# Performance work log

Measured on AMD Instinct MI355X. Metric: run time of the kernel, lower is better.

Reference implementation:

```python
import jax, jax.numpy as jnp
import numpy as np

N, G, H = 262144, 512, 16
EPS = 1e-5

Q_MAT = jnp.array([[0.0, 0.0, 1.0], [1.0, 0.0, 0.0], [0.0, 1.0, 0.0]], dtype=jnp.float32)
Q_TENSOR = jnp.kron(Q_MAT, Q_MAT)  # 9x9


def setup_inputs() -> dict:
    key = jax.random.key(0)
    ks = jax.random.split(key, 10)
    # sorted node->graph ids, every graph guaranteed non-empty
    gid = jnp.sort(jnp.concatenate([
        jnp.arange(G, dtype=jnp.int32),
        jax.random.randint(ks[0], (N - G,), 0, G, dtype=jnp.int32)]))
    return {
        'x00': jax.random.normal(ks[1], (N, 4 * H), jnp.float32),
        'x10': jax.random.normal(ks[2], (N, H, 3), jnp.float32),
        'x01': jax.random.normal(ks[3], (N, H, 3), jnp.float32),
        'x11': jax.random.normal(ks[4], (N, H, 9), jnp.float32),
        'pos': jax.random.normal(ks[5], (N, 6), jnp.float32),
        'graph_ids': gid,
        'num_graphs': G,
        'bn_gamma': jnp.ones((4 * H,), jnp.float32),
        'bn_beta': jnp.zeros((4 * H,), jnp.float32),
        'lin_w': jax.random.normal(ks[6], (3, 4 * H), jnp.float32) * 0.1,
        'lin_b': jnp.zeros((3,), jnp.float32),
        'w10': jax.random.normal(ks[7], (1, H), jnp.float32) * 0.3,
        'w01': jax.random.normal(ks[8], (1, H), jnp.float32) * 0.3,
        'w11': jax.random.normal(ks[9], (1, H), jnp.float32) * 0.3,
    }


def _graph_norm(x, seg, num_seg, gamma, beta):
    # per-graph mean/var normalization over nodes ('gn')
    cnt = jax.ops.segment_sum(jnp.ones((x.shape[0],), x.dtype), seg, num_segments=num_seg)
    cnt = jnp.maximum(cnt, 1.0)[:, None]
    mean = jax.ops.segment_sum(x, seg, num_segments=num_seg) / cnt
    var = jax.ops.segment_sum(x * x, seg, num_segments=num_seg) / cnt - mean * mean
    xn = (x - mean[seg]) * jax.lax.rsqrt(var[seg] + EPS)
    return xn * gamma + beta


def _segment_softmax(logits, seg, num_seg):
    m = jax.ops.segment_max(logits, seg, num_segments=num_seg)
    e = jnp.exp(logits - m[seg])
    s = jax.ops.segment_sum(e, seg, num_segments=num_seg)
    return e / s[seg]


def _project_r(r_vector):
    # SVD projection to nearest rotation (sign-corrected)
    norm = jnp.clip(jnp.linalg.norm(r_vector, axis=1, keepdims=True), 1e-5, None)
    r_vector = r_vector / jax.lax.stop_gradient(norm)  # norm is detached in torch
    # einops 'b (d c) -> b c d' with c=3
    r_ = jnp.transpose(r_vector.reshape(-1, 3, 3), (0, 2, 1))
    U, S, Vh = jnp.linalg.svd(r_, full_matrices=False)
    rot_pos = U @ Vh
    Vh_neg = Vh.at[:, 2, :].multiply(-1.0)
    rot_neg = U @ Vh_neg
    det = jnp.linalg.det(rot_pos)
    return jnp.where(det[:, None, None] > 0, rot_pos, rot_neg)


def reference(x00, x10, x01, x11, pos, graph_ids, num_graphs,
              bn_gamma, bn_beta, lin_w, lin_b, w10, w01, w11):
    seg = graph_ids
    Gn = num_graphs
    # BN('gn') + Linear -> 3 per-node logits
    xn = _graph_norm(x00, seg, Gn, bn_gamma, bn_beta)
    logits = xn @ lin_w.T + lin_b                       # [N,3]
    W = _segment_softmax(logits, seg, Gn)                # per-graph softmax over nodes
    w0, w1, w2 = W[:, 0:1], W[:, 1:2], W[:, 2:3]
    # weighted per-graph sums (dgl.sum_nodes)
    ab = jnp.concatenate([x10, x01], axis=-1)            # [N,H,6]
    mean_ab = jax.ops.segment_sum(ab * w1[:, :, None], seg, num_segments=Gn)   # [G,H,6]
    r_sum = jax.ops.segment_sum(x11 * w0[:, :, None], seg, num_segments=Gn)    # [G,H,9]
    m1m2 = jax.ops.segment_sum(pos * w2, seg, num_segments=Gn)                 # [G,6]
    m1, m2 = m1m2[:, 0:3], m1m2[:, 3:]
    # GLinear head: channel-mixing H -> 1 per degree type (no bias)
    out10 = jnp.einsum('oc,gcd->god', w10, mean_ab[:, :, :3])[:, 0, :]  # [G,3]
    out01 = jnp.einsum('oc,gcd->god', w01, mean_ab[:, :, 3:6])[:, 0, :]
    out11 = jnp.einsum('oc,gcd->god', w11, r_sum)[:, 0, :]              # [G,9]
    # permutation back to input frame
    r_vector = jnp.einsum('ij,gj->gi', Q_TENSOR, out11)
    trans_b = jnp.einsum('ij,gj->gi', Q_MAT, out01)
    trans_a = jnp.einsum('ij,gj->gi', Q_MAT, out10)
    rot_mat = _project_r(r_vector)
    t = m2 + trans_b - (rot_mat @ m1[..., None])[..., 0] - (rot_mat @ trans_a[..., None])[..., 0]
    return rot_mat, t, r_vector
```

## Files before the change

### kernel.cpp

```cpp
#include <hip/hip_runtime.h>
#include <cstdint>
#include <cstddef>

#define GG 512
#define NF 64
#define EPSF 1e-5f

__global__ __launch_bounds__(256) void k_stats(const float* __restrict__ x00, const int* __restrict__ gid,
                        float* __restrict__ gsum, float* __restrict__ gsq,
                        float* __restrict__ gcnt, int N, int nwave)
{
    int w = (blockIdx.x * blockDim.x + threadIdx.x) >> 6;
    if (w >= nwave) return;
    int lane = threadIdx.x & 63;
    long base = (long)w * 32;
    int gf = gid[base];
    int gl = gid[base + 31];
    if (gf == gl) {
        const float4* p = reinterpret_cast<const float4*>(x00 + base * NF) + lane;
        float s0=0,s1=0,s2=0,s3=0,q0=0,q1=0,q2=0,q3=0;
        #pragma unroll
        for (int k = 0; k < 8; ++k) {
            float4 v = p[k * 64];
            s0+=v.x; s1+=v.y; s2+=v.z; s3+=v.w;
            q0=fmaf(v.x,v.x,q0); q1=fmaf(v.y,v.y,q1); q2=fmaf(v.z,v.z,q2); q3=fmaf(v.w,v.w,q3);
        }
        #pragma unroll
        for (int m = 16; m < 64; m <<= 1) {
            s0+=__shfl_xor(s0,m); s1+=__shfl_xor(s1,m); s2+=__shfl_xor(s2,m); s3+=__shfl_xor(s3,m);
            q0+=__shfl_xor(q0,m); q1+=__shfl_xor(q1,m); q2+=__shfl_xor(q2,m); q3+=__shfl_xor(q3,m);
        }
        if (lane < 16) {
            float* ds = gsum + gf * NF + lane * 4;
            float* dq = gsq  + gf * NF + lane * 4;
            atomicAdd(ds+0,s0); atomicAdd(ds+1,s1); atomicAdd(ds+2,s2); atomicAdd(ds+3,s3);
            atomicAdd(dq+0,q0); atomicAdd(dq+1,q1); atomicAdd(dq+2,q2); atomicAdd(dq+3,q3);
        }
        if (lane == 0) atomicAdd(&gcnt[gf], 32.0f);
    } else {
        int myg = gid[base + (lane & 31)];
        int cur = gf;
        float s = 0.f, q = 0.f, cnt = 0.f;
        for (int k = 0; k < 32; ++k) {
            int g = __shfl(myg, k);
            if (g != cur) {
                atomicAdd(&gsum[cur * NF + lane], s);
                atomicAdd(&gsq [cur * NF + lane], q);
                if (lane == 0) atomicAdd(&gcnt[cur], cnt);
                s = q = cnt = 0.f; cur = g;
            }
            float v = x00[(base + k) * NF + lane];
            s += v; q = fmaf(v, v, q); cnt += 1.f;
        }
        atomicAdd(&gsum[cur * NF + lane], s);
        atomicAdd(&gsq [cur * NF + lane], q);
        if (lane == 0) atomicAdd(&gcnt[cur], cnt);
    }
}

__global__ void k_prep(const float* __restrict__ gsum, const float* __restrict__ gsq,
                       const float* __restrict__ gcnt,
                       const float* __restrict__ gamma, const float* __restrict__ beta,
                       const float* __restrict__ lin_w, const float* __restrict__ lin_b,
                       float* __restrict__ Aeff, float* __restrict__ Beff)
{
    int g = blockIdx.x;
    int c = threadIdx.x;
    float cnt = fmaxf(gcnt[g], 1.f);
    float mean = gsum[g * NF + c] / cnt;
    float var  = gsq [g * NF + c] / cnt - mean * mean;
    float rs = rsqrtf(var + EPSF);
    float ga = gamma[c], be = beta[c];
    #pragma unroll
    for (int j = 0; j < 3; ++j) {
        float wv = lin_w[j * NF + c];
        Aeff[((long)g * 3 + j) * NF + c] = rs * ga * wv;
        float term = (be - mean * rs * ga) * wv;
        #pragma unroll
        for (int m = 32; m; m >>= 1) term += __shfl_xor(term, m);
        if (c == 0) Beff[g * 3 + j] = term + lin_b[j];
    }
}

__global__ __launch_bounds__(128) void k_logits(const float* __restrict__ x00, const int* __restrict__ gid,
                         const float* __restrict__ pos,
                         const float* __restrict__ Aeff, const float* __restrict__ Beff,
                         float* __restrict__ ebp, float* __restrict__ accum, int N)
{
    __shared__ float T2[2][64 * 68];
    int wid = threadIdx.x >> 6;
    int lane = threadIdx.x & 63;
    long chunk = (long)blockIdx.x * 2 + wid;
    long base = chunk * 64;
    float* T = T2[wid];

    const float* src = x00 + base * NF;
    #pragma unroll
    for (int k = 0; k < 16; ++k) {
        int fl = k * 256 + lane * 4;
        float4 v = *reinterpret_cast<const float4*>(src + fl);
        int n = fl >> 6, c = fl & 63;
        *reinterpret_cast<float4*>(&T[n * 68 + c]) = v;
    }
    __syncthreads();

    int gf = gid[base], gl = gid[base + 63];
    float l0, l1, l2;
    int g_l;
    if (gf == gl) {
        g_l = gf;
        const float* ap = Aeff + (size_t)gf * 192;
        float a0a=0,a0b=0,a1a=0,a1b=0,a2a=0,a2b=0;
        #pragma unroll
        for (int t = 0; t < 16; ++t) {
            float4 xv = *reinterpret_cast<const float4*>(&T[lane * 68 + 4 * t]);
            float4 w0 = *reinterpret_cast<const float4*>(ap + 4 * t);
            float4 w1 = *reinterpret_cast<const float4*>(ap + 64 + 4 * t);
            float4 w2 = *reinterpret_cast<const float4*>(ap + 128 + 4 * t);
            a0a = fmaf(xv.x,w0.x,fmaf(xv.y,w0.y,a0a)); a0b = fmaf(xv.z,w0.z,fmaf(xv.w,w0.w,a0b));
            a1a = fmaf(xv.x,w1.x,fmaf(xv.y,w1.y,a1a)); a1b = fmaf(xv.z,w1.z,fmaf(xv.w,w1.w,a1b));
            a2a = fmaf(xv.x,w2.x,fmaf(xv.y,w2.y,a2a)); a2b = fmaf(xv.z,w2.z,fmaf(xv.w,w2.w,a2b));
        }
        l0 = a0a + a0b + Beff[gf*3+0];
        l1 = a1a + a1b + Beff[gf*3+1];
        l2 = a2a + a2b + Beff[gf*3+2];
    } else {
        g_l = gid[base + lane];
        const float* ap = Aeff + (size_t)g_l * 192;
        float a0=0,a1=0,a2=0;
        #pragma unroll
        for (int t = 0; t < 16; ++t) {
            float4 xv = *reinterpret_cast<const float4*>(&T[lane * 68 + 4 * t]);
            float4 w0 = *reinterpret_cast<const float4*>(ap + 4 * t);
            float4 w1 = *reinterpret_cast<const float4*>(ap + 64 + 4 * t);
            float4 w2 = *reinterpret_cast<const float4*>(ap + 128 + 4 * t);
            a0 = fmaf(xv.x,w0.x,fmaf(xv.y,w0.y,fmaf(xv.z,w0.z,fmaf(xv.w,w0.w,a0))));
            a1 = fmaf(xv.x,w1.x,fmaf(xv.y,w1.y,fmaf(xv.z,w1.z,fmaf(xv.w,w1.w,a1))));
            a2 = fmaf(xv.x,w2.x,fmaf(xv.y,w2.y,fmaf(xv.z,w2.z,fmaf(xv.w,w2.w,a2))));
        }
        l0 = a0 + Beff[g_l*3+0];
        l1 = a1 + Beff[g_l*3+1];
        l2 = a2 + Beff[g_l*3+2];
    }
    float e0 = expf(l0), e1 = expf(l1), e2 = expf(l2);
    long node = base + lane;
    ebp[node]            = e0;
    ebp[(long)N + node]  = e1;
    ebp[2L * N + node]   = e2;

    const float* pp = pos + node * 6;
    float2 v01 = *reinterpret_cast<const float2*>(pp);
    float2 v23 = *reinterpret_cast<const float2*>(pp + 2);
    float2 v45 = *reinterpret_cast<const float2*>(pp + 4);
    float p0 = v01.x*e2, p1 = v01.y*e2, p2 = v23.x*e2, p3 = v23.y*e2, p4 = v45.x*e2, p5 = v45.y*e2;
    if (gf == gl) {
        #pragma unroll
        for (int m = 1; m < 64; m <<= 1) {
            e0+=__shfl_xor(e0,m); e1+=__shfl_xor(e1,m); e2+=__shfl_xor(e2,m);
            p0+=__shfl_xor(p0,m); p1+=__shfl_xor(p1,m); p2+=__shfl_xor(p2,m);
            p3+=__shfl_xor(p3,m); p4+=__shfl_xor(p4,m); p5+=__shfl_xor(p5,m);
        }
        if (lane == 0) {
            float* dst = accum + (long)gf * 256;
            atomicAdd(dst+240,p0); atomicAdd(dst+241,p1); atomicAdd(dst+242,p2);
            atomicAdd(dst+243,p3); atomicAdd(dst+244,p4); atomicAdd(dst+245,p5);
            atomicAdd(dst+246,e0); atomicAdd(dst+247,e1); atomicAdd(dst+248,e2);
        }
    } else {
        float* dst = accum + (long)g_l * 256;
        atomicAdd(dst+240,p0); atomicAdd(dst+241,p1); atomicAdd(dst+242,p2);
        atomicAdd(dst+243,p3); atomicAdd(dst+244,p4); atomicAdd(dst+245,p5);
        atomicAdd(dst+246,e0); atomicAdd(dst+247,e1); atomicAdd(dst+248,e2);
    }
}

__global__ __launch_bounds__(256) void k_wsum(const float* __restrict__ x10, const float* __restrict__ x01,
                       const float* __restrict__ x11,
                       const float* __restrict__ ebp, const int* __restrict__ gid,
                       float* __restrict__ accum, int N, int nwave)
{
    int w = (blockIdx.x * blockDim.x + threadIdx.x) >> 6;
    if (w >= nwave) return;
    int lane = threadIdx.x & 63;
    long base = (long)w * 32;

    const float* p; long stride; const float* eb; int accOff; bool wr = true;
    if (lane < 12)      { p = x10 + lane * 4;        stride = 48;  eb = ebp + N; accOff = lane * 4; }
    else if (lane < 24) { p = x01 + (lane - 12) * 4; stride = 48;  eb = ebp + N; accOff = 48 + (lane - 12) * 4; }
    else if (lane < 60) { p = x11 + (lane - 24) * 4; stride = 144; eb = ebp;     accOff = 96 + (lane - 24) * 4; }
    else                { p = x11 + 140;             stride = 144; eb = ebp;     accOff = 0; wr = false; }

    int gf = gid[base], gl = gid[base + 31];
    float a0=0,a1=0,a2=0,a3=0;
    const float* pp = p + base * stride;
    const float* ep = eb + base;

    if (gf == gl) {
        #pragma unroll 8
        for (int k = 0; k < 32; ++k) {
            float e = ep[k];
            float4 v = *reinterpret_cast<const float4*>(pp + (long)k * stride);
            a0 = fmaf(v.x,e,a0); a1 = fmaf(v.y,e,a1); a2 = fmaf(v.z,e,a2); a3 = fmaf(v.w,e,a3);
        }
        if (wr) {
            float* dst = accum + (long)gf * 256 + accOff;
            atomicAdd(dst+0,a0); atomicAdd(dst+1,a1); atomicAdd(dst+2,a2); atomicAdd(dst+3,a3);
        }
    } else {
        int myg = gid[base + (lane & 31)];
        int cur = gf;
        for (int k = 0; k < 32; ++k) {
            int g = __shfl(myg, k);
            if (g != cur) {
                if (wr) {
                    float* dst = accum + (long)cur * 256 + accOff;
                    atomicAdd(dst+0,a0); atomicAdd(dst+1,a1); atomicAdd(dst+2,a2); atomicAdd(dst+3,a3);
                }
                a0=a1=a2=a3=0.f; cur = g;
            }
            float e = ep[k];
            float4 v = *reinterpret_cast<const float4*>(pp + (long)k * stride);
            a0 = fmaf(v.x,e,a0); a1 = fmaf(v.y,e,a1); a2 = fmaf(v.z,e,a2); a3 = fmaf(v.w,e,a3);
        }
        if (wr) {
            float* dst = accum + (long)cur * 256 + accOff;
            atomicAdd(dst+0,a0); atomicAdd(dst+1,a1); atomicAdd(dst+2,a2); atomicAdd(dst+3,a3);
        }
    }
}

#define JROT(p, q) do { \
    float apq_ = S[p][q]; \
    if (fabsf(apq_) > 1e-20f) { \
        float app_ = S[p][p], aqq_ = S[q][q]; \
        float tau_ = (aqq_ - app_) / (2.0f * apq_); \
        float tt_ = copysignf(1.0f, tau_) / (fabsf(tau_) + sqrtf(1.0f + tau_ * tau_)); \
        float cc_ = 1.0f / sqrtf(1.0f + tt_ * tt_); \
        float ssn_ = tt_ * cc_; \
        _Pragma("unroll") for (int kk = 0; kk < 3; ++kk) { \
            float skp = S[kk][p], skq = S[kk][q]; \
            S[kk][p] = cc_ * skp - ssn_ * skq; S[kk][q] = ssn_ * skp + cc_ * skq; } \
        _Pragma("unroll") for (int kk = 0; kk < 3; ++kk) { \
            float spk = S[p][kk], sqk = S[q][kk]; \
            S[p][kk] = cc_ * spk - ssn_ * sqk; S[q][kk] = ssn_ * spk + cc_ * sqk; } \
        _Pragma("unroll") for (int kk = 0; kk < 3; ++kk) { \
            float vkp = V[kk][p], vkq = V[kk][q]; \
            V[kk][p] = cc_ * vkp - ssn_ * vkq; V[kk][q] = ssn_ * vkp + cc_ * vkq; } \
    } \
} while (0)

__global__ void k_final(const float* __restrict__ accum,
                        const float* __restrict__ w10, const float* __restrict__ w01,
                        const float* __restrict__ w11, float* __restrict__ out)
{
    int g = blockIdx.x * blockDim.x + threadIdx.x;
    if (g >= GG) return;
    const float* A_ = accum + (long)g * 256;
    float s0 = A_[246], s1 = A_[247], s2 = A_[248];
    float i0 = 1.f / s0, i1 = 1.f / s1, i2 = 1.f / s2;

    float o10[3] = {0, 0, 0}, o01[3] = {0, 0, 0};
    float o11[9] = {0, 0, 0, 0, 0, 0, 0, 0, 0};
    #pragma unroll
    for (int c = 0; c < 16; ++c) {
        float wa = w10[c], wb = w01[c], wc = w11[c];
        #pragma unroll
        for (int d = 0; d < 3; ++d) o10[d] += wa * A_[c * 3 + d];
        #pragma unroll
        for (int d = 0; d < 3; ++d) o01[d] += wb * A_[48 + c * 3 + d];
        #pragma unroll
        for (int d = 0; d < 9; ++d) o11[d] += wc * A_[96 + c * 9 + d];
    }
    #pragma unroll
    for (int d = 0; d < 3; ++d) { o10[d] *= i1; o01[d] *= i1; }
    #pragma unroll
    for (int d = 0; d < 9; ++d) o11[d] *= i0;

    float m1v[3], m2v[3];
    #pragma unroll
    for (int d = 0; d < 3; ++d) { m1v[d] = A_[240 + d] * i2; m2v[d] = A_[243 + d] * i2; }

    const int sg0 = 2, sg1 = 0, sg2 = 1;
    int sig[3]; sig[0] = sg0; sig[1] = sg1; sig[2] = sg2;
    float rv[9];
    #pragma unroll
    for (int a = 0; a < 3; ++a)
        #pragma unroll
        for (int b = 0; b < 3; ++b)
            rv[a * 3 + b] = o11[sig[a] * 3 + sig[b]];
    float ta[3], tb[3];
    #pragma unroll
    for (int a = 0; a < 3; ++a) { ta[a] = o10[sig[a]]; tb[a] = o01[sig[a]]; }

    float nn = 0.f;
    #pragma unroll
    for (int k = 0; k < 9; ++k) nn += rv[k] * rv[k];
    float invn = 1.f / fmaxf(sqrtf(nn), 1e-5f);
    float M[3][3];
    #pragma unroll
    for (int a = 0; a < 3; ++a)
        #pragma unroll
        for (int b = 0; b < 3; ++b)
            M[a][b] = rv[b * 3 + a] * invn;

    float S[3][3], V[3][3];
    #pragma unroll
    for (int a = 0; a < 3; ++a)
        #pragma unroll
        for (int b = 0; b < 3; ++b) {
            float acc = 0.f;
            #pragma unroll
            for (int k = 0; k < 3; ++k) acc += M[k][a] * M[k][b];
            S[a][b] = acc;
            V[a][b] = (a == b) ? 1.f : 0.f;
        }
    for (int sw = 0; sw < 12; ++sw) { JROT(0, 1); JROT(0, 2); JROT(1, 2); }

    float l0 = S[0][0], l1 = S[1][1], l2 = S[2][2];
    float e0x = V[0][0], e0y = V[1][0], e0z = V[2][0];
    float e1x = V[0][1], e1y = V[1][1], e1z = V[2][1];
    float e2x = V[0][2], e2y = V[1][2], e2z = V[2][2];
    float tfl;
    if (l0 < l1) { tfl=l0;l0=l1;l1=tfl; tfl=e0x;e0x=e1x;e1x=tfl; tfl=e0y;e0y=e1y;e1y=tfl; tfl=e0z;e0z=e1z;e1z=tfl; }
    if (l0 < l2) { tfl=l0;l0=l2;l2=tfl; tfl=e0x;e0x=e2x;e2x=tfl; tfl=e0y;e0y=e2y;e2y=tfl; tfl=e0z;e0z=e2z;e2z=tfl; }
    if (l1 < l2) { tfl=l1;l1=l2;l2=tfl; tfl=e1x;e1x=e2x;e2x=tfl; tfl=e1y;e1y=e2y;e2y=tfl; tfl=e1z;e1z=e2z;e2z=tfl; }

    float c2x = e0y * e1z - e0z * e1y;
    float c2y = e0z * e1x - e0x * e1z;
    float c2z = e0x * e1y - e0y * e1x;
    float cn = rsqrtf(fmaxf(c2x * c2x + c2y * c2y + c2z * c2z, 1e-30f));
    c2x *= cn; c2y *= cn; c2z *= cn;

    float u0x = M[0][0] * e0x + M[0][1] * e0y + M[0][2] * e0z;
    float u0y = M[1][0] * e0x + M[1][1] * e0y + M[1][2] * e0z;
    float u0z = M[2][0] * e0x + M[2][1] * e0y + M[2][2] * e0z;
    float un = rsqrtf(fmaxf(u0x * u0x + u0y * u0y + u0z * u0z, 1e-30f));
    u0x *= un; u0y *= un; u0z *= un;
    float u1x = M[0][0] * e1x + M[0][1] * e1y + M[0][2] * e1z;
    float u1y = M[1][0] * e1x + M[1][1] * e1y + M[1][2] * e1z;
    float u1z = M[2][0] * e1x + M[2][1] * e1y + M[2][2] * e1z;
    float dp = u0x * u1x + u0y * u1y + u0z * u1z;
    u1x -= dp * u0x; u1y -= dp * u0y; u1z -= dp * u0z;
    un = rsqrtf(fmaxf(u1x * u1x + u1y * u1y + u1z * u1z, 1e-30f));
    u1x *= un; u1y *= un; u1z *= un;
    float u2x = u0y * u1z - u0z * u1y;
    float u2y = u0z * u1x - u0x * u1z;
    float u2z = u0x * u1y - u0y * u1x;

    float R[3][3];
    R[0][0] = u0x * e0x + u1x * e1x + u2x * c2x;
    R[0][1] = u0x * e0y + u1x * e1y + u2x * c2y;
    R[0][2] = u0x * e0z + u1x * e1z + u2x * c2z;
    R[1][0] = u0y * e0x + u1y * e1x + u2y * c2x;
    R[1][1] = u0y * e0y + u1y * e1y + u2y * c2y;
    R[1][2] = u0y * e0z + u1y * e1z + u2y * c2z;
    R[2][0] = u0z * e0x + u1z * e1x + u2z * c2x;
    R[2][1] = u0z * e0y + u1z * e1y + u2z * c2y;
    R[2][2] = u0z * e0z + u1z * e1z + u2z * c2z;

    float tv[3];
    #pragma unroll
    for (int a = 0; a < 3; ++a) {
        float acc = m2v[a] + tb[a];
        #pragma unroll
        for (int b = 0; b < 3; ++b) acc -= R[a][b] * (m1v[b] + ta[b]);
        tv[a] = acc;
    }

    #pragma unroll
    for (int k = 0; k < 9; ++k) out[(long)g * 9 + k] = R[k / 3][k % 3];
    #pragma unroll
    for (int a = 0; a < 3; ++a) out[(long)GG * 9 + (long)g * 3 + a] = tv[a];
    #pragma unroll
    for (int k = 0; k < 9; ++k) out[(long)GG * 12 + (long)g * 9 + k] = rv[k];
}

extern "C" void kernel_launch(void* const* d_in, const int* in_sizes, int n_in,
                              void* d_out, int out_size, void* d_ws, size_t ws_size,
                              hipStream_t stream)
{
    const float* x00   = (const float*)d_in[0];
    const float* x10   = (const float*)d_in[1];
    const float* x01   = (const float*)d_in[2];
    const float* x11   = (const float*)d_in[3];
    const float* pos   = (const float*)d_in[4];
    const int*   gid   = (const int*)d_in[5];
    const float* gamma = (const float*)d_in[7];
    const float* beta  = (const float*)d_in[8];
    const float* lin_w = (const float*)d_in[9];
    const float* lin_b = (const float*)d_in[10];
    const float* w10   = (const float*)d_in[11];
    const float* w01   = (const float*)d_in[12];
    const float* w11   = (const float*)d_in[13];
    float* out = (float*)d_out;

    const int N = in_sizes[0] / NF;

    float* ws = (float*)d_ws;
    float* gsum  = ws;
    float* gsq   = gsum + GG * 64;
    float* gcnt  = gsq + GG * 64;
    float* accum = gcnt + GG;
    float* Aeff  = accum + GG * 256;
    float* Beff  = Aeff + GG * 192;
    float* ebp   = Beff + GG * 3;

    size_t zeroBytes = (size_t)(GG * 64 * 2 + GG + GG * 256) * sizeof(float);
    hipMemsetAsync(d_ws, 0, zeroBytes, stream);

    int nwave32 = N / 32;
    int blocks32 = nwave32 / 4;
    int blocksLg = (N / 64) / 2;

    k_stats <<<blocks32, 256, 0, stream>>>(x00, gid, gsum, gsq, gcnt, N, nwave32);
    k_prep  <<<GG, 64, 0, stream>>>(gsum, gsq, gcnt, gamma, beta, lin_w, lin_b, Aeff, Beff);
    k_logits<<<blocksLg, 128, 0, stream>>>(x00, gid, pos, Aeff, Beff, ebp, accum, N);
    k_wsum  <<<blocks32, 256, 0, stream>>>(x10, x01, x11, ebp, gid, accum, N, nwave32);
    k_final <<<(GG + 63) / 64, 64, 0, stream>>>(accum, w10, w01, w11, out);
}
```

Before: 191.5 us.

## Fuse GLinear channel mix into wsum, double rows per wave, use unsafe atomics

The channel-mixing weights w10/w01/w11 are folded into k_wsum. Each wave now reduces its 16 channels through shared memory down to 15 outputs before issuing atomics, which shrinks the per-graph accumulator from 256 floats to 32. The stats and wsum kernels now process 64 rows per wave instead of 32, and all float atomics go through unsafeAtomicAdd to get the hardware FP32 atomic. Together these cut atomic traffic and the memset size, at the cost of an LDS round-trip per flush and removal of the bounds checks on wave count.

```diff
diff --git a/kernel.cpp b/kernel.cpp
--- a/kernel.cpp
+++ b/kernel.cpp
@@ -6,21 +6,24 @@
 #define NF 64
 #define EPSF 1e-5f
 
+__device__ __forceinline__ void atomAddF(float* p, float v) {
+    unsafeAtomicAdd(p, v);
+}
+
 __global__ __launch_bounds__(256) void k_stats(const float* __restrict__ x00, const int* __restrict__ gid,
                         float* __restrict__ gsum, float* __restrict__ gsq,
-                        float* __restrict__ gcnt, int N, int nwave)
+                        float* __restrict__ gcnt, int N)
 {
     int w = (blockIdx.x * blockDim.x + threadIdx.x) >> 6;
-    if (w >= nwave) return;
     int lane = threadIdx.x & 63;
-    long base = (long)w * 32;
+    long base = (long)w * 64;
     int gf = gid[base];
-    int gl = gid[base + 31];
+    int gl = gid[base + 63];
     if (gf == gl) {
         const float4* p = reinterpret_cast<const float4*>(x00 + base * NF) + lane;
         float s0=0,s1=0,s2=0,s3=0,q0=0,q1=0,q2=0,q3=0;
         #pragma unroll
-        for (int k = 0; k < 8; ++k) {
+        for (int k = 0; k < 16; ++k) {
             float4 v = p[k * 64];
             s0+=v.x; s1+=v.y; s2+=v.z; s3+=v.w;
             q0=fmaf(v.x,v.x,q0); q1=fmaf(v.y,v.y,q1); q2=fmaf(v.z,v.z,q2); q3=fmaf(v.w,v.w,q3);
@@ -33,28 +36,28 @@
         if (lane < 16) {
             float* ds = gsum + gf * NF + lane * 4;
             float* dq = gsq  + gf * NF + lane * 4;
-            atomicAdd(ds+0,s0); atomicAdd(ds+1,s1); atomicAdd(ds+2,s2); atomicAdd(ds+3,s3);
-            atomicAdd(dq+0,q0); atomicAdd(dq+1,q1); atomicAdd(dq+2,q2); atomicAdd(dq+3,q3);
-        }
-        if (lane == 0) atomicAdd(&gcnt[gf], 32.0f);
+            atomAddF(ds+0,s0); atomAddF(ds+1,s1); atomAddF(ds+2,s2); atomAddF(ds+3,s3);
+            atomAddF(dq+0,q0); atomAddF(dq+1,q1); atomAddF(dq+2,q2); atomAddF(dq+3,q3);
+        }
+        if (lane == 0) atomAddF(&gcnt[gf], 64.0f);
     } else {
-        int myg = gid[base + (lane & 31)];
+        int myg = gid[base + lane];
         int cur = gf;
         float s = 0.f, q = 0.f, cnt = 0.f;
-        for (int k = 0; k < 32; ++k) {
+        for (int k = 0; k < 64; ++k) {
             int g = __shfl(myg, k);
             if (g != cur) {
-                atomicAdd(&gsum[cur * NF + lane], s);
-                atomicAdd(&gsq [cur * NF + lane], q);
-                if (lane == 0) atomicAdd(&gcnt[cur], cnt);
+                atomAddF(&gsum[cur * NF + lane], s);
+                atomAddF(&gsq [cur * NF + lane], q);
+                if (lane == 0) atomAddF(&gcnt[cur], cnt);
                 s = q = cnt = 0.f; cur = g;
             }
             float v = x00[(base + k) * NF + lane];
             s += v; q = fmaf(v, v, q); cnt += 1.f;
         }
-        atomicAdd(&gsum[cur * NF + lane], s);
-        atomicAdd(&gsq [cur * NF + lane], q);
-        if (lane == 0) atomicAdd(&gcnt[cur], cnt);
+        atomAddF(&gsum[cur * NF + lane], s);
+        atomAddF(&gsq [cur * NF + lane], q);
+        if (lane == 0) atomAddF(&gcnt[cur], cnt);
     }
 }
 
@@ -161,71 +164,96 @@
             p3+=__shfl_xor(p3,m); p4+=__shfl_xor(p4,m); p5+=__shfl_xor(p5,m);
         }
         if (lane == 0) {
-            float* dst = accum + (long)gf * 256;
-            atomicAdd(dst+240,p0); atomicAdd(dst+241,p1); atomicAdd(dst+242,p2);
-            atomicAdd(dst+243,p3); atomicAdd(dst+244,p4); atomicAdd(dst+245,p5);
-            atomicAdd(dst+246,e0); atomicAdd(dst+247,e1); atomicAdd(dst+248,e2);
+            float* dst = accum + (long)gf * 32;
+            atomAddF(dst+16,p0); atomAddF(dst+17,p1); atomAddF(dst+18,p2);
+            atomAddF(dst+19,p3); atomAddF(dst+20,p4); atomAddF(dst+21,p5);
+            atomAddF(dst+22,e0); atomAddF(dst+23,e1); atomAddF(dst+24,e2);
         }
     } else {
-        float* dst = accum + (long)g_l * 256;
-        atomicAdd(dst+240,p0); atomicAdd(dst+241,p1); atomicAdd(dst+242,p2);
-        atomicAdd(dst+243,p3); atomicAdd(dst+244,p4); atomicAdd(dst+245,p5);
-        atomicAdd(dst+246,e0); atomicAdd(dst+247,e1); atomicAdd(dst+248,e2);
+        float* dst = accum + (long)g_l * 32;
+        atomAddF(dst+16,p0); atomAddF(dst+17,p1); atomAddF(dst+18,p2);
+        atomAddF(dst+19,p3); atomAddF(dst+20,p4); atomAddF(dst+21,p5);
+        atomAddF(dst+22,e0); atomAddF(dst+23,e1); atomAddF(dst+24,e2);
     }
 }
 
 __global__ __launch_bounds__(256) void k_wsum(const float* __restrict__ x10, const float* __restrict__ x01,
                        const float* __restrict__ x11,
                        const float* __restrict__ ebp, const int* __restrict__ gid,
-                       float* __restrict__ accum, int N, int nwave)
-{
+                       const float* __restrict__ w10, const float* __restrict__ w01,
+                       const float* __restrict__ w11,
+                       float* __restrict__ accum, int N)
+{
+    __shared__ float Tb[4][240];
+    int wid = threadIdx.x >> 6;
     int w = (blockIdx.x * blockDim.x + threadIdx.x) >> 6;
-    if (w >= nwave) return;
     int lane = threadIdx.x & 63;
-    long base = (long)w * 32;
+    long base = (long)w * 64;
+    float* T = Tb[wid];
 
     const float* p; long stride; const float* eb; int accOff; bool wr = true;
-    if (lane < 12)      { p = x10 + lane * 4;        stride = 48;  eb = ebp + N; accOff = lane * 4; }
-    else if (lane < 24) { p = x01 + (lane - 12) * 4; stride = 48;  eb = ebp + N; accOff = 48 + (lane - 12) * 4; }
-    else if (lane < 60) { p = x11 + (lane - 24) * 4; stride = 144; eb = ebp;     accOff = 96 + (lane - 24) * 4; }
-    else                { p = x11 + 140;             stride = 144; eb = ebp;     accOff = 0; wr = false; }
-
-    int gf = gid[base], gl = gid[base + 31];
+    float wt0, wt1, wt2, wt3;
+    if (lane < 12) {
+        p = x10 + lane * 4; stride = 48; eb = ebp + N; accOff = lane * 4;
+        int f = lane * 4;
+        wt0 = w10[f/3]; wt1 = w10[(f+1)/3]; wt2 = w10[(f+2)/3]; wt3 = w10[(f+3)/3];
+    } else if (lane < 24) {
+        p = x01 + (lane - 12) * 4; stride = 48; eb = ebp + N; accOff = 48 + (lane - 12) * 4;
+        int f = (lane - 12) * 4;
+        wt0 = w01[f/3]; wt1 = w01[(f+1)/3]; wt2 = w01[(f+2)/3]; wt3 = w01[(f+3)/3];
+    } else if (lane < 60) {
+        p = x11 + (lane - 24) * 4; stride = 144; eb = ebp; accOff = 96 + (lane - 24) * 4;
+        int f = (lane - 24) * 4;
+        wt0 = w11[f/9]; wt1 = w11[(f+1)/9]; wt2 = w11[(f+2)/9]; wt3 = w11[(f+3)/9];
+    } else {
+        p = x11 + 140; stride = 144; eb = ebp; accOff = 0; wr = false;
+        wt0 = wt1 = wt2 = wt3 = 0.f;
+    }
+
     float a0=0,a1=0,a2=0,a3=0;
     const float* pp = p + base * stride;
     const float* ep = eb + base;
 
+    auto flush = [&](int g) {
+        asm volatile("" ::: "memory");
+        if (wr) {
+            T[accOff+0] = a0*wt0; T[accOff+1] = a1*wt1;
+            T[accOff+2] = a2*wt2; T[accOff+3] = a3*wt3;
+        }
+        asm volatile("s_waitcnt lgkmcnt(0)" ::: "memory");
+        if (lane < 15) {
+            int off, strd;
+            if (lane < 3)      { off = lane;            strd = 3; }
+            else if (lane < 6) { off = 48 + (lane - 3); strd = 3; }
+            else               { off = 96 + (lane - 6); strd = 9; }
+            float s = 0.f;
+            #pragma unroll
+            for (int c = 0; c < 16; ++c) s += T[off + c * strd];
+            atomAddF(accum + (long)g * 32 + lane, s);
+        }
+        asm volatile("s_waitcnt lgkmcnt(0)" ::: "memory");
+    };
+
+    int gf = gid[base], gl = gid[base + 63];
     if (gf == gl) {
         #pragma unroll 8
-        for (int k = 0; k < 32; ++k) {
+        for (int k = 0; k < 64; ++k) {
             float e = ep[k];
             float4 v = *reinterpret_cast<const float4*>(pp + (long)k * stride);
             a0 = fmaf(v.x,e,a0); a1 = fmaf(v.y,e,a1); a2 = fmaf(v.z,e,a2); a3 = fmaf(v.w,e,a3);
         }
-        if (wr) {
-            float* dst = accum + (long)gf * 256 + accOff;
-            atomicAdd(dst+0,a0); atomicAdd(dst+1,a1); atomicAdd(dst+2,a2); atomicAdd(dst+3,a3);
-        }
+        flush(gf);
     } else {
-        int myg = gid[base + (lane & 31)];
+        int myg = gid[base + lane];
         int cur = gf;
-        for (int k = 0; k < 32; ++k) {
+        for (int k = 0; k < 64; ++k) {
             int g = __shfl(myg, k);
-            if (g != cur) {
-                if (wr) {
-                    float* dst = accum + (long)cur * 256 + accOff;
-                    atomicAdd(dst+0,a0); atomicAdd(dst+1,a1); atomicAdd(dst+2,a2); atomicAdd(dst+3,a3);
-                }
-                a0=a1=a2=a3=0.f; cur = g;
-            }
+            if (g != cur) { flush(cur); a0=a1=a2=a3=0.f; cur = g; }
             float e = ep[k];
             float4 v = *reinterpret_cast<const float4*>(pp + (long)k * stride);
             a0 = fmaf(v.x,e,a0); a1 = fmaf(v.y,e,a1); a2 = fmaf(v.z,e,a2); a3 = fmaf(v.w,e,a3);
         }
-        if (wr) {
-            float* dst = accum + (long)cur * 256 + accOff;
-            atomicAdd(dst+0,a0); atomicAdd(dst+1,a1); atomicAdd(dst+2,a2); atomicAdd(dst+3,a3);
-        }
+        flush(cur);
     }
 }
 
@@ -249,39 +277,24 @@
     } \
 } while (0)
 
-__global__ void k_final(const float* __restrict__ accum,
-                        const float* __restrict__ w10, const float* __restrict__ w01,
-                        const float* __restrict__ w11, float* __restrict__ out)
+__global__ void k_final(const float* __restrict__ accum, float* __restrict__ out)
 {
     int g = blockIdx.x * blockDim.x + threadIdx.x;
     if (g >= GG) return;
-    const float* A_ = accum + (long)g * 256;
-    float s0 = A_[246], s1 = A_[247], s2 = A_[248];
-    float i0 = 1.f / s0, i1 = 1.f / s1, i2 = 1.f / s2;
-
-    float o10[3] = {0, 0, 0}, o01[3] = {0, 0, 0};
-    float o11[9] = {0, 0, 0, 0, 0, 0, 0, 0, 0};
-    #pragma unroll
-    for (int c = 0; c < 16; ++c) {
-        float wa = w10[c], wb = w01[c], wc = w11[c];
-        #pragma unroll
-        for (int d = 0; d < 3; ++d) o10[d] += wa * A_[c * 3 + d];
-        #pragma unroll
-        for (int d = 0; d < 3; ++d) o01[d] += wb * A_[48 + c * 3 + d];
-        #pragma unroll
-        for (int d = 0; d < 9; ++d) o11[d] += wc * A_[96 + c * 9 + d];
-    }
-    #pragma unroll
-    for (int d = 0; d < 3; ++d) { o10[d] *= i1; o01[d] *= i1; }
-    #pragma unroll
-    for (int d = 0; d < 9; ++d) o11[d] *= i0;
+    const float* A_ = accum + (long)g * 32;
+    float i0 = 1.f / A_[22], i1 = 1.f / A_[23], i2 = 1.f / A_[24];
+
+    float o10[3], o01[3], o11[9];
+    #pragma unroll
+    for (int d = 0; d < 3; ++d) { o10[d] = A_[d] * i1; o01[d] = A_[3 + d] * i1; }
+    #pragma unroll
+    for (int d = 0; d < 9; ++d) o11[d] = A_[6 + d] * i0;
 
     float m1v[3], m2v[3];
     #pragma unroll
-    for (int d = 0; d < 3; ++d) { m1v[d] = A_[240 + d] * i2; m2v[d] = A_[243 + d] * i2; }
-
-    const int sg0 = 2, sg1 = 0, sg2 = 1;
-    int sig[3]; sig[0] = sg0; sig[1] = sg1; sig[2] = sg2;
+    for (int d = 0; d < 3; ++d) { m1v[d] = A_[16 + d] * i2; m2v[d] = A_[19 + d] * i2; }
+
+    int sig[3]; sig[0] = 2; sig[1] = 0; sig[2] = 1;
     float rv[9];
     #pragma unroll
     for (int a = 0; a < 3; ++a)
@@ -401,20 +414,20 @@
     float* gsq   = gsum + GG * 64;
     float* gcnt  = gsq + GG * 64;
     float* accum = gcnt + GG;
-    float* Aeff  = accum + GG * 256;
+    float* Aeff  = accum + GG * 32;
     float* Beff  = Aeff + GG * 192;
     float* ebp   = Beff + GG * 3;
 
-    size_t zeroBytes = (size_t)(GG * 64 * 2 + GG + GG * 256) * sizeof(float);
+    size_t zeroBytes = (size_t)(GG * 64 * 2 + GG + GG * 32) * sizeof(float);
     hipMemsetAsync(d_ws, 0, zeroBytes, stream);
 
-    int nwave32 = N / 32;
-    int blocks32 = nwave32 / 4;
+    int nwave64 = N / 64;
+    int blocks64 = nwave64 / 4;
     int blocksLg = (N / 64) / 2;
 
-    k_stats <<<blocks32, 256, 0, stream>>>(x00, gid, gsum, gsq, gcnt, N, nwave32);
+    k_stats <<<blocks64, 256, 0, stream>>>(x00, gid, gsum, gsq, gcnt, N);
     k_prep  <<<GG, 64, 0, stream>>>(gsum, gsq, gcnt, gamma, beta, lin_w, lin_b, Aeff, Beff);
     k_logits<<<blocksLg, 128, 0, stream>>>(x00, gid, pos, Aeff, Beff, ebp, accum, N);
-    k_wsum  <<<blocks32, 256, 0, stream>>>(x10, x01, x11, ebp, gid, accum, N, nwave32);
-    k_final <<<(GG + 63) / 64, 64, 0, stream>>>(accum, w10, w01, w11, out);
-}
+    k_wsum  <<<blocks64, 256, 0, stream>>>(x10, x01, x11, ebp, gid, w10, w01, w11, accum, N);
+    k_final <<<(GG + 63) / 64, 64, 0, stream>>>(accum, out);
+}
```

Measured after the change: 187.5 us. 1.02x faster.
